# Optimization experiments

Hardware: AMD Instinct MI355X
Metric: run time of the kernel (lower is better)

## Reference

```python
import jax, jax.numpy as jnp
import numpy as np

B, T, D, E = 4, 1024, 1024, 8
HD = 4 * D  # hdim = 4*dim


def setup_inputs() -> dict:
    key = jax.random.key(0)
    k1, k2, k3, k4 = jax.random.split(key, 4)
    std = 0.5 * D ** (-0.5)
    bound = (3.0 ** 0.5) * std
    x = jax.random.normal(k1, (B, T, D), dtype=jnp.float32)
    # router zero-init in source; use small random weights so routing is non-degenerate
    router_w = jax.random.normal(k2, (E, D), dtype=jnp.float32) * 0.02
    expert_fc = jax.random.uniform(k3, (E, D, HD), dtype=jnp.float32, minval=-bound, maxval=bound)
    # proj zero-init in source; use small random so output/backward are non-trivial
    expert_proj = jax.random.normal(k4, (E, D, HD), dtype=jnp.float32) * 0.02
    return {"x": x, "router_w": router_w, "expert_fc": expert_fc, "expert_proj": expert_proj}


def reference(x, router_w, expert_fc, expert_proj):
    # router: Linear(dim, E, bias=False) -> logits [B,T,E]
    logits = jnp.einsum('btd,ed->bte', x, router_w)
    probs = jax.nn.softmax(logits, axis=-1)
    expert_ids = jnp.argmax(probs, axis=-1)  # [B,T]; top-1 (max) routing
    # NOTE: source computes expert_weights (max prob) but does NOT use it in combine.
    mask = jax.nn.one_hot(expert_ids, E, dtype=x.dtype)  # [B,T,E]
    # Dense all-experts compute (faithful to source): h = x @ fc (F.linear with fc.T)
    h = jnp.einsum('btd,edh->ebth', x, expert_fc)
    h = jnp.square(jax.nn.relu(h))  # relu(h)**2
    # expert_output = h @ proj.T (F.linear with proj [dim, hdim])
    out_e = jnp.einsum('ebth,edh->ebtd', h, expert_proj)
    # masked combine: sum_e out_e * (ids == e)
    output = jnp.einsum('ebtd,bte->btd', out_e, mask)
    return output
```

## Files before the change

kernel.cpp:

```cpp
#include <hip/hip_runtime.h>
#include <hip/hip_bf16.h>
#include <stdint.h>

#define NE 8
#define DIM 1024
#define HDIM 4096
#define NTOK 4096
#define KSPLIT 4
#define MAXT 24
#define NT 16

typedef unsigned short ushort_t;
typedef __attribute__((ext_vector_type(4))) float f32x4;
typedef __attribute__((ext_vector_type(8))) short bf16x8;
typedef __attribute__((ext_vector_type(8))) ushort_t u16x8;

#define WAITV(n) asm volatile("s_waitcnt vmcnt(" #n ")" ::: "memory")
#define WAITL0() asm volatile("s_waitcnt lgkmcnt(0)" ::: "memory")
#define SCHEDB() __builtin_amdgcn_sched_barrier(0)
#define BARRIER() __builtin_amdgcn_s_barrier()

__device__ __forceinline__ ushort_t f2b(float f) {
  union { float f; unsigned u; } c; c.f = f;
  unsigned u = c.u;
  return (ushort_t)((u + 0x7fffu + ((u >> 16) & 1u)) >> 16);
}

__device__ __forceinline__ unsigned pk2(float a, float b) {
  union { float f; unsigned u; } x, y; x.f = a; y.f = b;
  return __builtin_amdgcn_perm(y.u, x.u, 0x07060302);
}

__device__ __forceinline__ void gl2lds16(const void* g, void* l) {
  __builtin_amdgcn_global_load_lds(
      (__attribute__((address_space(1))) void*)g,
      (__attribute__((address_space(3))) void*)l, 16, 0, 0);
}

#define PH_MFMA(mh, nh)                                                     \
  { __builtin_amdgcn_s_setprio(1);                                          \
    _Pragma("unroll")                                                       \
    for (int i2 = 0; i2 < 4; ++i2) {                                        \
      _Pragma("unroll")                                                     \
      for (int j2 = 0; j2 < 2; ++j2) {                                      \
        _Pragma("unroll")                                                   \
        for (int kk = 0; kk < 2; ++kk)                                      \
          acc[(mh)*4 + i2][(nh)*2 + j2] =                                   \
            __builtin_amdgcn_mfma_f32_16x16x32_bf16(                        \
              af[i2][kk], bf[(nh)*2 + j2][kk],                              \
              acc[(mh)*4 + i2][(nh)*2 + j2], 0, 0, 0);                      \
      }                                                                     \
    }                                                                       \
    __builtin_amdgcn_s_setprio(0); }

#define LOAD_AF(mh)                                                         \
  { _Pragma("unroll")                                                       \
    for (int i2 = 0; i2 < 4; ++i2) {                                        \
      _Pragma("unroll")                                                     \
      for (int kk = 0; kk < 2; ++kk)                                        \
        af[i2][kk] = *(const bf16x8*)&pA[aBase + ((mh)*64 + i2*16)*64 + ck[kk]]; \
    } }
#define LOAD_BF(nh)                                                         \
  { _Pragma("unroll")                                                       \
    for (int j2 = 0; j2 < 2; ++j2) {                                        \
      _Pragma("unroll")                                                     \
      for (int kk = 0; kk < 2; ++kk)                                        \
        bf[(nh)*2 + j2][kk] = *(const bf16x8*)&pB[bBase + (((nh)*2 + j2)*16)*64 + ck[kk]]; \
    } }

__global__ __launch_bounds__(256) void router_kernel(
    const float* __restrict__ x, const float* __restrict__ rw,
    int* __restrict__ eid, int* __restrict__ rank, int* __restrict__ cnt) {
  __shared__ float w[NE * 1028];
  for (int i = threadIdx.x; i < NE * DIM; i += 256) {
    int e = i >> 10, d = i & 1023;
    w[e * 1028 + d] = rw[i];
  }
  __syncthreads();
  int grp = threadIdx.x >> 3;
  int e = threadIdx.x & 7;
  int t = blockIdx.x * 32 + grp;
  const float4* xr = (const float4*)(x + (size_t)t * DIM);
  const float4* wr = (const float4*)(w + e * 1028);
  float acc = 0.f;
#pragma unroll 4
  for (int i = 0; i < DIM / 4; ++i) {
    float4 xv = xr[i], wv = wr[i];
    acc += xv.x * wv.x + xv.y * wv.y + xv.z * wv.z + xv.w * wv.w;
  }
  float v = acc; int ie = e;
#pragma unroll
  for (int m = 4; m; m >>= 1) {
    float ov = __shfl_xor(v, m, 8);
    int oi = __shfl_xor(ie, m, 8);
    if (ov > v || (ov == v && oi < ie)) { v = ov; ie = oi; }
  }
  if (e == 0) {
    eid[t] = ie;
    rank[t] = atomicAdd(&cnt[ie], 1);
  }
}

__global__ void scan_kernel(const int* __restrict__ cnt, int* __restrict__ offs,
                            int* __restrict__ tile_e, int* __restrict__ tile_m,
                            int* __restrict__ ntiles) {
  if (threadIdx.x == 0) {
    int s = 0, nt = 0;
    for (int e = 0; e < NE; ++e) {
      offs[e] = s;
      int c = cnt[e];
      for (int m = 0; m < c; m += 256) { tile_e[nt] = e; tile_m[nt] = m; ++nt; }
      s += c;
    }
    offs[NE] = s;
    *ntiles = nt;
  }
}

__global__ __launch_bounds__(256) void gather_kernel(
    const float* __restrict__ x, const int* __restrict__ eid,
    const int* __restrict__ rank, const int* __restrict__ offs,
    int* __restrict__ sorted, ushort_t* __restrict__ Xg) {
  int t = blockIdx.x;
  int e = eid[t];
  int pos = offs[e] + rank[t];
  if (threadIdx.x == 0) sorted[pos] = t;
  int i = threadIdx.x;
  float4 v = ((const float4*)(x + (size_t)t * DIM))[i];
  ushort4 o = make_ushort4(f2b(v.x), f2b(v.y), f2b(v.z), f2b(v.w));
  *(ushort4*)(Xg + (size_t)pos * DIM + i * 4) = o;
}

__global__ __launch_bounds__(256) void transpose_fc_kernel(
    const float* __restrict__ fc, ushort_t* __restrict__ fct) {
  __shared__ float tile[64][68];
  int e = blockIdx.z;
  int h0 = blockIdx.x * 64, d0 = blockIdx.y * 64;
  int tid = threadIdx.x;
  int rr = tid >> 4;
  int cc = (tid & 15) * 4;
  const float* src = fc + ((size_t)e * DIM + d0 + rr) * HDIM + h0 + cc;
#pragma unroll
  for (int i = 0; i < 4; ++i) {
    float4 v = *(const float4*)(src + (size_t)(i * 16) * HDIM);
    *(float4*)&tile[rr + i * 16][cc] = v;
  }
  __syncthreads();
  int hr = tid >> 2;
  int dseg = (tid & 3) * 16;
  union { ushort_t s[16]; u16x8 v[2]; } o;
#pragma unroll
  for (int j = 0; j < 16; ++j) o.s[j] = f2b(tile[dseg + j][hr]);
  ushort_t* dst = fct + ((size_t)e * HDIM + h0 + hr) * DIM + d0 + dseg;
  *(u16x8*)dst = o.v[0];
  *(u16x8*)(dst + 8) = o.v[1];
}

__global__ __launch_bounds__(512, 2) void gemm1_kernel(
    const ushort_t* __restrict__ Xg, const ushort_t* __restrict__ fct,
    const int* __restrict__ offs, const int* __restrict__ tile_e,
    const int* __restrict__ tile_m, const int* __restrict__ ntiles,
    ushort_t* __restrict__ H) {
  __shared__ ushort_t As[2][16384];
  __shared__ ushort_t Bs[2][16384];

  int lin = blockIdx.x + 16 * blockIdx.y;
  int sw = (lin & 7) * 48 + (lin >> 3);
  int bx = sw & 15, by = sw >> 4;
  if (by >= *ntiles) return;

  int e = tile_e[by];
  int mb = tile_m[by];
  int m0 = offs[e];
  int Me = offs[e + 1] - m0;
  int n0 = bx * 256;

  int tid = threadIdx.x;
  int wave = tid >> 6;
  int lane = tid & 63;
  int fr = lane & 15, kq = lane >> 4;
  int wr = wave & 1, wc = wave >> 1;

  int swk = ((tid & 7) ^ ((tid >> 3) & 7)) * 8;
  const ushort_t* aSrc[4]; const ushort_t* bSrc[4];
#pragma unroll
  for (int c = 0; c < 4; ++c) {
    int r = c * 64 + (tid >> 3);
    int rg = mb + r; if (rg >= Me) rg = Me - 1;
    aSrc[c] = Xg + (size_t)(m0 + rg) * DIM + swk;
    bSrc[c] = fct + ((size_t)e * HDIM + n0 + r) * DIM + swk;
  }
  int sdst = wave * 512;

  int aBase = (wr * 128 + fr) * 64;
  int bBase = (wc * 64 + fr) * 64;
  int ck[2] = { (kq ^ (fr & 7)) * 8, ((4 + kq) ^ (fr & 7)) * 8 };

  f32x4 acc[8][4] = {};
  bf16x8 af[4][2], bf[4][2];

  auto stage = [&](int p, int X) __attribute__((always_inline)) {
    int ko = X * 64;
#pragma unroll
    for (int c = 0; c < 4; ++c)
      gl2lds16(aSrc[c] + ko, &As[p][c * 4096 + sdst]);
#pragma unroll
    for (int c = 0; c < 4; ++c)
      gl2lds16(bSrc[c] + ko, &Bs[p][c * 4096 + sdst]);
  };

  stage(0, 0);
  stage(1, 1);
  WAITV(8);

  for (int T = 0; T < NT; ++T) {
    const int p = T & 1;
    const ushort_t* pA = As[p];
    const ushort_t* pB = Bs[p];
    BARRIER(); SCHEDB();
    LOAD_AF(0); LOAD_BF(0);
    WAITL0(); SCHEDB();
    PH_MFMA(0, 0);
    LOAD_BF(1);
    WAITL0(); SCHEDB();
    PH_MFMA(0, 1);
    LOAD_AF(1);
    WAITL0(); SCHEDB();
    PH_MFMA(1, 0);
    BARRIER(); SCHEDB();
    if (T + 2 < NT) { stage(p, T + 2); WAITV(8); }
    else if (T + 1 < NT) { WAITV(0); }
    PH_MFMA(1, 1);
  }

  int cq = kq * 4;
#pragma unroll
  for (int i = 0; i < 8; ++i) {
#pragma unroll
    for (int r = 0; r < 4; ++r) {
      int rl = wr * 128 + i * 16 + cq + r;
      int rg = mb + rl;
      if (rg < Me) {
        ushort_t* dst = H + (size_t)(m0 + rg) * HDIM + n0 + wc * 64 + fr;
#pragma unroll
        for (int j = 0; j < 4; ++j) {
          float v = acc[i][j][r];
          v = fmaxf(v, 0.f);
          dst[j * 16] = f2b(v * v);
        }
      }
    }
  }
}

__global__ __launch_bounds__(512, 2) void gemm2_kernel(
    const ushort_t* __restrict__ Hm, const float* __restrict__ pj,
    const int* __restrict__ offs, const int* __restrict__ tile_e,
    const int* __restrict__ tile_m, const int* __restrict__ ntiles,
    float* __restrict__ P) {
  __shared__ ushort_t As[2][16384];
  __shared__ ushort_t Bs[2][16384];

  int lin = blockIdx.x + 4 * (blockIdx.y + MAXT * blockIdx.z);
  int sw = (lin & 7) * 48 + (lin >> 3);
  int bx = sw & 3;
  int t2 = sw >> 2;
  int by = t2 % MAXT, bz = t2 / MAXT;
  if (by >= *ntiles) return;

  int e = tile_e[by];
  int mb = tile_m[by];
  int ks = bz;
  int m0 = offs[e];
  int Me = offs[e + 1] - m0;
  int n0 = bx * 256;
  int kbeg = ks * (HDIM / KSPLIT);

  int tid = threadIdx.x;
  int wave = tid >> 6;
  int lane = tid & 63;
  int fr = lane & 15, kq = lane >> 4;
  int wr = wave & 1, wc = wave >> 1;

  int swk = ((tid & 7) ^ ((tid >> 3) & 7)) * 8;
  const ushort_t* aSrc[4];
  const float* bSrc[4];
  int bDst[4];
#pragma unroll
  for (int c = 0; c < 4; ++c) {
    int r = c * 64 + (tid >> 3);
    int rg = mb + r; if (rg >= Me) rg = Me - 1;
    aSrc[c] = Hm + (size_t)(m0 + rg) * HDIM + kbeg + swk;
    bSrc[c] = pj + ((size_t)e * DIM + n0 + r) * HDIM + kbeg + (tid & 7) * 8;
    bDst[c] = r * 64 + swk;
  }
  int sdst = wave * 512;

  int aBase = (wr * 128 + fr) * 64;
  int bBase = (wc * 64 + fr) * 64;
  int ck[2] = { (kq ^ (fr & 7)) * 8, ((4 + kq) ^ (fr & 7)) * 8 };

  f32x4 acc[8][4] = {};
  bf16x8 af[4][2], bf[4][2];
  float4 bv[8];

  auto loadB = [&](int X) __attribute__((always_inline)) {
    int ko = X * 64;
#pragma unroll
    for (int c = 0; c < 4; ++c) {
      bv[2 * c]     = *(const float4*)(bSrc[c] + ko);
      bv[2 * c + 1] = *(const float4*)(bSrc[c] + ko + 4);
    }
  };
  auto writeB = [&](int pb) __attribute__((always_inline)) {
#pragma unroll
    for (int c = 0; c < 4; ++c) {
      union { unsigned u[4]; bf16x8 v; } w;
      w.u[0] = pk2(bv[2*c].x, bv[2*c].y);     w.u[1] = pk2(bv[2*c].z, bv[2*c].w);
      w.u[2] = pk2(bv[2*c+1].x, bv[2*c+1].y); w.u[3] = pk2(bv[2*c+1].z, bv[2*c+1].w);
      *(bf16x8*)&Bs[pb][bDst[c]] = w.v;
    }
  };
  auto stageA = [&](int p, int X) __attribute__((always_inline)) {
    int ko = X * 64;
#pragma unroll
    for (int c = 0; c < 4; ++c)
      gl2lds16(aSrc[c] + ko, &As[p][c * 4096 + sdst]);
  };

  loadB(0); stageA(0, 0);
  WAITV(4);
  writeB(0);
  loadB(1); stageA(1, 1);
  WAITV(4);
  writeB(1);
  WAITL0();

  for (int T = 0; T < NT; ++T) {
    const int p = T & 1;
    const ushort_t* pA = As[p];
    const ushort_t* pB = Bs[p];
    BARRIER(); SCHEDB();
    if (T >= 1 && T + 1 < NT) loadB(T + 1);
    LOAD_AF(0); LOAD_BF(0);
    WAITL0(); SCHEDB();
    PH_MFMA(0, 0);
    LOAD_BF(1);
    WAITL0(); SCHEDB();
    PH_MFMA(0, 1);
    LOAD_AF(1);
    WAITL0(); SCHEDB();
    PH_MFMA(1, 0);
    BARRIER(); SCHEDB();
    if (T + 2 < NT) stageA(p, T + 2);
    if (T + 1 < NT) { if (T + 2 < NT) { WAITV(4); } else { WAITV(0); } }
    if (T >= 1 && T + 1 < NT) { writeB(p ^ 1); WAITL0(); }
    PH_MFMA(1, 1);
  }

  int cq = kq * 4;
#pragma unroll
  for (int i = 0; i < 8; ++i) {
#pragma unroll
    for (int r = 0; r < 4; ++r) {
      int rl = wr * 128 + i * 16 + cq + r;
      int rg = mb + rl;
      if (rg < Me) {
        float* dst = P + ((size_t)ks * NTOK + (m0 + rg)) * DIM + n0 + wc * 64 + fr;
#pragma unroll
        for (int j = 0; j < 4; ++j) dst[j * 16] = acc[i][j][r];
      }
    }
  }
}

__global__ __launch_bounds__(256) void reduce_kernel(
    const float* __restrict__ P, const int* __restrict__ sorted,
    float* __restrict__ out) {
  int pos = blockIdx.x;
  int tok = sorted[pos];
  int i = threadIdx.x;
  size_t base = (size_t)pos * DIM + i * 4;
  const size_t S = (size_t)NTOK * DIM;
  f32x4 s = *(const f32x4*)(P + base) + *(const f32x4*)(P + S + base) +
            *(const f32x4*)(P + 2 * S + base) + *(const f32x4*)(P + 3 * S + base);
  *(f32x4*)(out + (size_t)tok * DIM + i * 4) = s;
}

extern "C" void kernel_launch(void* const* d_in, const int* in_sizes, int n_in,
                              void* d_out, int out_size, void* d_ws, size_t ws_size,
                              hipStream_t stream) {
  const float* x  = (const float*)d_in[0];
  const float* rw = (const float*)d_in[1];
  const float* fc = (const float*)d_in[2];
  const float* pj = (const float*)d_in[3];
  float* out = (float*)d_out;
  char* ws = (char*)d_ws;

  int* eid        = (int*)(ws + 0x0000);
  int* rank       = (int*)(ws + 0x4000);
  int* cnt        = (int*)(ws + 0x8000);
  int* offs       = (int*)(ws + 0x8100);
  int* tile_e     = (int*)(ws + 0x8200);
  int* tile_m     = (int*)(ws + 0x8600);
  int* ntiles     = (int*)(ws + 0x8a00);
  int* sorted     = (int*)(ws + 0x9000);
  ushort_t* Xg    = (ushort_t*)(ws + 0x10000);
  ushort_t* H     = (ushort_t*)(ws + 0x810000);
  ushort_t* W     = (ushort_t*)(ws + 0x2810000);
  float* P        = (float*)W;

  hipMemsetAsync(cnt, 0, 32, stream);
  router_kernel<<<NTOK / 32, 256, 0, stream>>>(x, rw, eid, rank, cnt);
  scan_kernel<<<1, 64, 0, stream>>>(cnt, offs, tile_e, tile_m, ntiles);
  gather_kernel<<<NTOK, 256, 0, stream>>>(x, eid, rank, offs, sorted, Xg);
  transpose_fc_kernel<<<dim3(HDIM / 64, DIM / 64, NE), 256, 0, stream>>>(fc, W);
  gemm1_kernel<<<dim3(HDIM / 256, MAXT), 512, 0, stream>>>(Xg, W, offs, tile_e, tile_m, ntiles, H);
  gemm2_kernel<<<dim3(DIM / 256, MAXT, KSPLIT), 512, 0, stream>>>(H, pj, offs, tile_e, tile_m, ntiles, P);
  reduce_kernel<<<NTOK, 256, 0, stream>>>(P, sorted, out);
}
```

Baseline: 498.6 us.

## Restructure GEMM pipeline with split stages, pre-cast proj to bf16, atomic fallback

Both GEMMs now use a shared main loop that splits global-to-LDS staging into halves interleaved with the MFMA phases, unrolled by two with extra barriers. A separate kernel casts expert_proj to bf16 up front, so gemm2 loads B directly into LDS instead of converting fp32 in registers. When the workspace is too small, gemm2 adds its partial sums into the output with atomics and skips the reduce kernel. The cast costs an extra pass over the 128MB proj tensor, and the added barriers may slow the loop.

```diff
diff --git a/kernel.cpp b/kernel.cpp
--- a/kernel.cpp
+++ b/kernel.cpp
@@ -17,6 +17,7 @@
 
 #define WAITV(n) asm volatile("s_waitcnt vmcnt(" #n ")" ::: "memory")
 #define WAITL0() asm volatile("s_waitcnt lgkmcnt(0)" ::: "memory")
+#define WAITL8() asm volatile("s_waitcnt lgkmcnt(8)" ::: "memory")
 #define SCHEDB() __builtin_amdgcn_sched_barrier(0)
 #define BARRIER() __builtin_amdgcn_s_barrier()
 
@@ -24,11 +25,6 @@
   union { float f; unsigned u; } c; c.f = f;
   unsigned u = c.u;
   return (ushort_t)((u + 0x7fffu + ((u >> 16) & 1u)) >> 16);
-}
-
-__device__ __forceinline__ unsigned pk2(float a, float b) {
-  union { float f; unsigned u; } x, y; x.f = a; y.f = b;
-  return __builtin_amdgcn_perm(y.u, x.u, 0x07060302);
 }
 
 __device__ __forceinline__ void gl2lds16(const void* g, void* l) {
@@ -156,6 +152,80 @@
   *(u16x8*)(dst + 8) = o.v[1];
 }
 
+__global__ __launch_bounds__(256) void cast_pj_kernel(
+    const float* __restrict__ pj, ushort_t* __restrict__ pjb) {
+  const size_t total = (size_t)NE * DIM * HDIM;
+  size_t stride = (size_t)gridDim.x * 256 * 8;
+  for (size_t i = ((size_t)blockIdx.x * 256 + threadIdx.x) * 8; i < total; i += stride) {
+    f32x4 a = *(const f32x4*)(pj + i);
+    f32x4 b = *(const f32x4*)(pj + i + 4);
+    union { ushort_t s[8]; u16x8 v; } o;
+    o.s[0] = f2b(a[0]); o.s[1] = f2b(a[1]); o.s[2] = f2b(a[2]); o.s[3] = f2b(a[3]);
+    o.s[4] = f2b(b[0]); o.s[5] = f2b(b[1]); o.s[6] = f2b(b[2]); o.s[7] = f2b(b[3]);
+    *(u16x8*)(pjb + i) = o.v;
+  }
+}
+
+#define GEMM_MAIN_LOOP()                                                    \
+  stB(0, 0, 0); stB(0, 0, 1); stA(0, 0, 0); stA(0, 0, 1);                   \
+  stB(1, 1, 0); stB(1, 1, 1); stA(1, 1, 0);                                 \
+  WAITV(6);                                                                 \
+  BARRIER();                                                                \
+  _Pragma("unroll 1")                                                       \
+  for (int T = 0; T < NT; T += 2) {                                         \
+    { const ushort_t* pA = As[0]; const ushort_t* pB = Bs[0];               \
+                                                                   \
+      LOAD_AF(0); LOAD_BF(0);                                               \
+      stA(1, T + 1, 1);                                                     \
+      WAITL8(); SCHEDB();                                                   \
+      BARRIER(); WAITL0(); SCHEDB();                                        \
+      PH_MFMA(0, 0);                                                        \
+      BARRIER();                                                            \
+                                                                   \
+      LOAD_BF(1);                                                           \
+      BARRIER(); WAITL0(); SCHEDB();                                        \
+      PH_MFMA(0, 1);                                                        \
+      BARRIER();                                                            \
+                                                                   \
+      LOAD_AF(1);                                                           \
+      if (T + 2 < NT) stB(0, T + 2, 0);                                     \
+      BARRIER(); WAITL0(); SCHEDB();                                        \
+      PH_MFMA(1, 0);                                                        \
+      BARRIER();                                                            \
+                                                                   \
+      if (T + 2 < NT) { stB(0, T + 2, 1); stA(0, T + 2, 0); WAITV(6); }     \
+      else            { WAITV(0); }                                         \
+      BARRIER(); SCHEDB();                                                  \
+      PH_MFMA(1, 1);                                                        \
+      BARRIER();                                                            \
+    }                                                                       \
+    { const ushort_t* pA = As[1]; const ushort_t* pB = Bs[1];               \
+                                                                   \
+      LOAD_AF(0); LOAD_BF(0);                                               \
+      if (T + 2 < NT) stA(0, T + 2, 1);                                     \
+      WAITL8(); SCHEDB();                                                   \
+      BARRIER(); WAITL0(); SCHEDB();                                        \
+      PH_MFMA(0, 0);                                                        \
+      BARRIER();                                                            \
+                                                                   \
+      LOAD_BF(1);                                                           \
+      BARRIER(); WAITL0(); SCHEDB();                                        \
+      PH_MFMA(0, 1);                                                        \
+      BARRIER();                                                            \
+                                                                   \
+      LOAD_AF(1);                                                           \
+      if (T + 3 < NT) stB(1, T + 3, 0);                                     \
+      BARRIER(); WAITL0(); SCHEDB();                                        \
+      PH_MFMA(1, 0);                                                        \
+      BARRIER();                                                            \
+                                                                   \
+      if (T + 3 < NT) { stB(1, T + 3, 1); stA(1, T + 3, 0); WAITV(6); }     \
+      BARRIER(); SCHEDB();                                                  \
+      PH_MFMA(1, 1);                                                        \
+      BARRIER();                                                            \
+    }                                                                       \
+  }
+
 __global__ __launch_bounds__(512, 2) void gemm1_kernel(
     const ushort_t* __restrict__ Xg, const ushort_t* __restrict__ fct,
     const int* __restrict__ offs, const int* __restrict__ tile_e,
@@ -199,39 +269,18 @@
   f32x4 acc[8][4] = {};
   bf16x8 af[4][2], bf[4][2];
 
-  auto stage = [&](int p, int X) __attribute__((always_inline)) {
+  auto stA = [&](int p, int X, int h) __attribute__((always_inline)) {
     int ko = X * 64;
-#pragma unroll
-    for (int c = 0; c < 4; ++c)
-      gl2lds16(aSrc[c] + ko, &As[p][c * 4096 + sdst]);
-#pragma unroll
-    for (int c = 0; c < 4; ++c)
-      gl2lds16(bSrc[c] + ko, &Bs[p][c * 4096 + sdst]);
+    gl2lds16(aSrc[2 * h] + ko,     &As[p][(2 * h) * 4096 + sdst]);
+    gl2lds16(aSrc[2 * h + 1] + ko, &As[p][(2 * h + 1) * 4096 + sdst]);
   };
-
-  stage(0, 0);
-  stage(1, 1);
-  WAITV(8);
-
-  for (int T = 0; T < NT; ++T) {
-    const int p = T & 1;
-    const ushort_t* pA = As[p];
-    const ushort_t* pB = Bs[p];
-    BARRIER(); SCHEDB();
-    LOAD_AF(0); LOAD_BF(0);
-    WAITL0(); SCHEDB();
-    PH_MFMA(0, 0);
-    LOAD_BF(1);
-    WAITL0(); SCHEDB();
-    PH_MFMA(0, 1);
-    LOAD_AF(1);
-    WAITL0(); SCHEDB();
-    PH_MFMA(1, 0);
-    BARRIER(); SCHEDB();
-    if (T + 2 < NT) { stage(p, T + 2); WAITV(8); }
-    else if (T + 1 < NT) { WAITV(0); }
-    PH_MFMA(1, 1);
-  }
+  auto stB = [&](int p, int X, int h) __attribute__((always_inline)) {
+    int ko = X * 64;
+    gl2lds16(bSrc[2 * h] + ko,     &Bs[p][(2 * h) * 4096 + sdst]);
+    gl2lds16(bSrc[2 * h + 1] + ko, &Bs[p][(2 * h + 1) * 4096 + sdst]);
+  };
+
+  GEMM_MAIN_LOOP();
 
   int cq = kq * 4;
 #pragma unroll
@@ -254,10 +303,10 @@
 }
 
 __global__ __launch_bounds__(512, 2) void gemm2_kernel(
-    const ushort_t* __restrict__ Hm, const float* __restrict__ pj,
+    const ushort_t* __restrict__ Hm, const ushort_t* __restrict__ pjb,
     const int* __restrict__ offs, const int* __restrict__ tile_e,
     const int* __restrict__ tile_m, const int* __restrict__ ntiles,
-    float* __restrict__ P) {
+    const int* __restrict__ sorted, float* P, float* __restrict__ out) {
   __shared__ ushort_t As[2][16384];
   __shared__ ushort_t Bs[2][16384];
 
@@ -283,16 +332,13 @@
   int wr = wave & 1, wc = wave >> 1;
 
   int swk = ((tid & 7) ^ ((tid >> 3) & 7)) * 8;
-  const ushort_t* aSrc[4];
-  const float* bSrc[4];
-  int bDst[4];
+  const ushort_t* aSrc[4]; const ushort_t* bSrc[4];
 #pragma unroll
   for (int c = 0; c < 4; ++c) {
     int r = c * 64 + (tid >> 3);
     int rg = mb + r; if (rg >= Me) rg = Me - 1;
     aSrc[c] = Hm + (size_t)(m0 + rg) * HDIM + kbeg + swk;
-    bSrc[c] = pj + ((size_t)e * DIM + n0 + r) * HDIM + kbeg + (tid & 7) * 8;
-    bDst[c] = r * 64 + swk;
+    bSrc[c] = pjb + ((size_t)e * DIM + n0 + r) * HDIM + kbeg + swk;
   }
   int sdst = wave * 512;
 
@@ -302,73 +348,48 @@
 
   f32x4 acc[8][4] = {};
   bf16x8 af[4][2], bf[4][2];
-  float4 bv[8];
-
-  auto loadB = [&](int X) __attribute__((always_inline)) {
+
+  auto stA = [&](int p, int X, int h) __attribute__((always_inline)) {
     int ko = X * 64;
-#pragma unroll
-    for (int c = 0; c < 4; ++c) {
-      bv[2 * c]     = *(const float4*)(bSrc[c] + ko);
-      bv[2 * c + 1] = *(const float4*)(bSrc[c] + ko + 4);
+    gl2lds16(aSrc[2 * h] + ko,     &As[p][(2 * h) * 4096 + sdst]);
+    gl2lds16(aSrc[2 * h + 1] + ko, &As[p][(2 * h + 1) * 4096 + sdst]);
+  };
+  auto stB = [&](int p, int X, int h) __attribute__((always_inline)) {
+    int ko = X * 64;
+    gl2lds16(bSrc[2 * h] + ko,     &Bs[p][(2 * h) * 4096 + sdst]);
+    gl2lds16(bSrc[2 * h + 1] + ko, &Bs[p][(2 * h + 1) * 4096 + sdst]);
+  };
+
+  GEMM_MAIN_LOOP();
+
+  int cq = kq * 4;
+  if (P) {
+#pragma unroll
+    for (int i = 0; i < 8; ++i) {
+#pragma unroll
+      for (int r = 0; r < 4; ++r) {
+        int rl = wr * 128 + i * 16 + cq + r;
+        int rg = mb + rl;
+        if (rg < Me) {
+          float* dst = P + ((size_t)ks * NTOK + (m0 + rg)) * DIM + n0 + wc * 64 + fr;
+#pragma unroll
+          for (int j = 0; j < 4; ++j) dst[j * 16] = acc[i][j][r];
+        }
+      }
     }
-  };
-  auto writeB = [&](int pb) __attribute__((always_inline)) {
-#pragma unroll
-    for (int c = 0; c < 4; ++c) {
-      union { unsigned u[4]; bf16x8 v; } w;
-      w.u[0] = pk2(bv[2*c].x, bv[2*c].y);     w.u[1] = pk2(bv[2*c].z, bv[2*c].w);
-      w.u[2] = pk2(bv[2*c+1].x, bv[2*c+1].y); w.u[3] = pk2(bv[2*c+1].z, bv[2*c+1].w);
-      *(bf16x8*)&Bs[pb][bDst[c]] = w.v;
-    }
-  };
-  auto stageA = [&](int p, int X) __attribute__((always_inline)) {
-    int ko = X * 64;
-#pragma unroll
-    for (int c = 0; c < 4; ++c)
-      gl2lds16(aSrc[c] + ko, &As[p][c * 4096 + sdst]);
-  };
-
-  loadB(0); stageA(0, 0);
-  WAITV(4);
-  writeB(0);
-  loadB(1); stageA(1, 1);
-  WAITV(4);
-  writeB(1);
-  WAITL0();
-
-  for (int T = 0; T < NT; ++T) {
-    const int p = T & 1;
-    const ushort_t* pA = As[p];
-    const ushort_t* pB = Bs[p];
-    BARRIER(); SCHEDB();
-    if (T >= 1 && T + 1 < NT) loadB(T + 1);
-    LOAD_AF(0); LOAD_BF(0);
-    WAITL0(); SCHEDB();
-    PH_MFMA(0, 0);
-    LOAD_BF(1);
-    WAITL0(); SCHEDB();
-    PH_MFMA(0, 1);
-    LOAD_AF(1);
-    WAITL0(); SCHEDB();
-    PH_MFMA(1, 0);
-    BARRIER(); SCHEDB();
-    if (T + 2 < NT) stageA(p, T + 2);
-    if (T + 1 < NT) { if (T + 2 < NT) { WAITV(4); } else { WAITV(0); } }
-    if (T >= 1 && T + 1 < NT) { writeB(p ^ 1); WAITL0(); }
-    PH_MFMA(1, 1);
-  }
-
-  int cq = kq * 4;
-#pragma unroll
-  for (int i = 0; i < 8; ++i) {
-#pragma unroll
-    for (int r = 0; r < 4; ++r) {
-      int rl = wr * 128 + i * 16 + cq + r;
-      int rg = mb + rl;
-      if (rg < Me) {
-        float* dst = P + ((size_t)ks * NTOK + (m0 + rg)) * DIM + n0 + wc * 64 + fr;
-#pragma unroll
-        for (int j = 0; j < 4; ++j) dst[j * 16] = acc[i][j][r];
+  } else {
+#pragma unroll
+    for (int i = 0; i < 8; ++i) {
+#pragma unroll
+      for (int r = 0; r < 4; ++r) {
+        int rl = wr * 128 + i * 16 + cq + r;
+        int rg = mb + rl;
+        if (rg < Me) {
+          int tok = sorted[m0 + rg];
+          float* dst = out + (size_t)tok * DIM + n0 + wc * 64 + fr;
+#pragma unroll
+          for (int j = 0; j < 4; ++j) atomicAdd(&dst[j * 16], acc[i][j][r]);
+        }
       }
     }
   }
@@ -408,14 +429,21 @@
   ushort_t* Xg    = (ushort_t*)(ws + 0x10000);
   ushort_t* H     = (ushort_t*)(ws + 0x810000);
   ushort_t* W     = (ushort_t*)(ws + 0x2810000);
-  float* P        = (float*)W;
+
+  const size_t pOff = 0x6810000ULL;
+  const size_t pBytes = (size_t)KSPLIT * NTOK * DIM * sizeof(float);
+  bool bigws = ws_size >= pOff + pBytes;
+  float* P = bigws ? (float*)(ws + pOff) : nullptr;
 
   hipMemsetAsync(cnt, 0, 32, stream);
+  if (!bigws) hipMemsetAsync(out, 0, (size_t)NTOK * DIM * sizeof(float), stream);
   router_kernel<<<NTOK / 32, 256, 0, stream>>>(x, rw, eid, rank, cnt);
   scan_kernel<<<1, 64, 0, stream>>>(cnt, offs, tile_e, tile_m, ntiles);
   gather_kernel<<<NTOK, 256, 0, stream>>>(x, eid, rank, offs, sorted, Xg);
   transpose_fc_kernel<<<dim3(HDIM / 64, DIM / 64, NE), 256, 0, stream>>>(fc, W);
   gemm1_kernel<<<dim3(HDIM / 256, MAXT), 512, 0, stream>>>(Xg, W, offs, tile_e, tile_m, ntiles, H);
-  gemm2_kernel<<<dim3(DIM / 256, MAXT, KSPLIT), 512, 0, stream>>>(H, pj, offs, tile_e, tile_m, ntiles, P);
-  reduce_kernel<<<NTOK, 256, 0, stream>>>(P, sorted, out);
-}
+  cast_pj_kernel<<<4096, 256, 0, stream>>>(pj, W);
+  gemm2_kernel<<<dim3(DIM / 256, MAXT, KSPLIT), 512, 0, stream>>>(
+      H, W, offs, tile_e, tile_m, ntiles, sorted, P, out);
+  if (bigws) reduce_kernel<<<NTOK, 256, 0, stream>>>(P, sorted, out);
+}
```

After: 503.7 us. About the same (+1.0%).
